# Performance work log

Measured on AMD Instinct MI355X. Metric: run time of the kernel, lower is better.

## Reference

```python
import jax, jax.numpy as jnp
import numpy as np

B, T, C, H = 2, 2048, 1024, 16  # batch, seq (== block_size), n_embd, n_head
HD = C // H  # head dim


def setup_inputs() -> dict:
    key = jax.random.key(0)
    k1, k2, k3 = jax.random.split(key, 3)
    x = jax.random.normal(k1, (B, T, C), dtype=jnp.float32)
    w_attn = jax.random.normal(k2, (C, 3 * C), dtype=jnp.float32) * (1.0 / np.sqrt(C))
    b_attn = jnp.zeros((3 * C,), dtype=jnp.float32)
    w_proj = jax.random.normal(k3, (C, C), dtype=jnp.float32) * (1.0 / np.sqrt(C))
    b_proj = jnp.zeros((C,), dtype=jnp.float32)
    return {"x": x, "w_attn": w_attn, "b_attn": b_attn, "w_proj": w_proj, "b_proj": b_proj}


def reference(x, w_attn, b_attn, w_proj, b_proj):
    # qkv projection: [B,T,3C]
    qkv = x @ w_attn + b_attn
    q, k, v = jnp.split(qkv, 3, axis=-1)
    # -> [B,H,T,HD]
    def to_heads(t):
        return t.reshape(B, T, H, HD).transpose(0, 2, 1, 3)
    q, k, v = to_heads(q), to_heads(k), to_heads(v)
    scale = 1.0 / np.sqrt(HD).astype(np.float32)
    # att: [B,H,T,T]
    att = jnp.einsum("bhqd,bhkd->bhqk", q, k) * scale
    causal = jnp.tril(jnp.ones((T, T), dtype=bool))
    att = jnp.where(causal[None, None], att, -jnp.inf)
    att = jax.nn.softmax(att, axis=-1)
    # y: [B,H,T,HD] -> [B,T,C]
    y = jnp.einsum("bhqk,bhkd->bhqd", att, v)
    y = y.transpose(0, 2, 1, 3).reshape(B, T, C)
    return y @ w_proj + b_proj
```

## Files before the change

kernel.cpp:

```cpp
#include <hip/hip_runtime.h>
#include <stdint.h>

#define Bb 2
#define Tt 2048
#define Cc 1024
#define Hh 16
#define HD 64
#define C3 3072

typedef __bf16 bf16x8 __attribute__((ext_vector_type(8)));
typedef float  f32x4  __attribute__((ext_vector_type(4)));
typedef unsigned short u16;
typedef u16 u16x8 __attribute__((ext_vector_type(8)));
typedef u16 u16x4 __attribute__((ext_vector_type(4)));

#define SCALE2 0.18033688f

__device__ __forceinline__ u16 f2bf(float f) {
  union { float f; unsigned u; } v; v.f = f;
  return (u16)((v.u + 0x7fffu + ((v.u >> 16) & 1u)) >> 16);
}
__device__ __forceinline__ float bf2f(u16 a) {
  union { unsigned u; float f; } v; v.u = ((unsigned)a) << 16; return v.f;
}

__device__ __forceinline__ void gl2lds16(const void* g, void* s) {
  __builtin_amdgcn_global_load_lds(
      (__attribute__((address_space(1))) void*)(g),
      (__attribute__((address_space(3))) void*)(s), 16, 0, 0);
}

__device__ __forceinline__ bf16x8 ldb8(const u16* p) {
  return __builtin_bit_cast(bf16x8, *(const u16x8*)p);
}

__global__ __launch_bounds__(256)
void prep_kernel(const float* __restrict__ x, const float* __restrict__ w_attn,
                 const float* __restrict__ w_proj, u16* __restrict__ xb,
                 u16* __restrict__ wat, u16* __restrict__ wpt) {
  __shared__ u16 tile[64][65];
  const int blk = blockIdx.x;
  const int tid = threadIdx.x;
  if (blk < 4096) {
    int i = blk * 256 + tid;
    float4 v = ((const float4*)x)[i];
    u16x4 o = { f2bf(v.x), f2bf(v.y), f2bf(v.z), f2bf(v.w) };
    ((u16x4*)xb)[i] = o;
    return;
  }
  const float* in; u16* out; int R, C, c0, r0;
  if (blk < 4096 + 768) {
    int t = blk - 4096;
    in = w_attn; out = wat; R = 1024; C = 3072;
    c0 = (t % 48) * 64; r0 = (t / 48) * 64;
  } else {
    int t = blk - 4864;
    in = w_proj; out = wpt; R = 1024; C = 1024;
    c0 = (t & 15) * 64; r0 = (t >> 4) * 64;
  }
  int xx = tid & 63, yy = tid >> 6;
  #pragma unroll
  for (int rr = yy; rr < 64; rr += 4)
    tile[rr][xx] = f2bf(in[(size_t)(r0 + rr) * C + c0 + xx]);
  __syncthreads();
  #pragma unroll
  for (int rr = yy; rr < 64; rr += 4)
    out[(size_t)(c0 + rr) * R + r0 + xx] = tile[xx][rr];
}

template <int MODE, int BN>
__global__ __launch_bounds__(256, 4)
void gemm_bt(const u16* __restrict__ A, const u16* __restrict__ Bt,
             const float* __restrict__ bias, void* __restrict__ Cout,
             u16* __restrict__ Vt, int M, int N, int K) {
  __shared__ u16 As[2][128 * 32];
  __shared__ u16 Bs[2][BN * 32];
  constexpr int JT = BN / 32;
  const int tid = threadIdx.x;
  const int ln  = tid & 63;
  const int w   = tid >> 6;
  const int wm  = w >> 1, wn = w & 1;
  const int l15 = ln & 15, lq = ln >> 4;
  const int swz2 = (l15 >> 1) & 3;
  const int m0 = blockIdx.y * 128, n0 = blockIdx.x * BN;

  int aoff[2], boff[BN / 128 + 1];
  #pragma unroll
  for (int i = 0; i < 2; ++i) {
    int s = i * 256 + tid;
    int row = s >> 2, cg = (s & 3) ^ ((s >> 3) & 3);
    aoff[i] = (m0 + row) * K + cg * 8;
  }
  #pragma unroll
  for (int i = 0; i < BN / 128 + 1; ++i) {
    int s = i * 256 + tid;
    int row = s >> 2, cg = (s & 3) ^ ((s >> 3) & 3);
    boff[i] = (n0 + row) * K + cg * 8;
  }

  f32x4 acc[4][JT];
  #pragma unroll
  for (int i = 0; i < 4; ++i)
    #pragma unroll
    for (int j = 0; j < JT; ++j)
      acc[i][j] = (f32x4){0.f, 0.f, 0.f, 0.f};

  const int NK = K >> 5;
  #pragma unroll
  for (int i = 0; i < 2; ++i)
    gl2lds16(A + aoff[i], (char*)As[0] + (size_t)(i * 256 + w * 64) * 16);
  #pragma unroll
  for (int i = 0; i < BN / 128 + 1; ++i)
    gl2lds16(Bt + boff[i], (char*)Bs[0] + (size_t)(i * 256 + w * 64) * 16);

  for (int it = 0; it < NK; ++it) {
    const int p = it & 1;
    __syncthreads();
    if (it + 1 < NK) {
      const int k0 = (it + 1) * 32;
      #pragma unroll
      for (int i = 0; i < 2; ++i)
        gl2lds16(A + aoff[i] + k0, (char*)As[p ^ 1] + (size_t)(i * 256 + w * 64) * 16);
      #pragma unroll
      for (int i = 0; i < BN / 128 + 1; ++i)
        gl2lds16(Bt + boff[i] + k0, (char*)Bs[p ^ 1] + (size_t)(i * 256 + w * 64) * 16);
    }
    const u16* AsB = As[p];
    const u16* BsB = Bs[p];
    bf16x8 af[4], bfr[JT];
    #pragma unroll
    for (int i = 0; i < 4; ++i)
      af[i] = ldb8(&AsB[(wm * 64 + i * 16 + l15) * 32 + ((lq ^ swz2) * 8)]);
    #pragma unroll
    for (int j = 0; j < JT; ++j)
      bfr[j] = ldb8(&BsB[(wn * (BN / 2) + j * 16 + l15) * 32 + ((lq ^ swz2) * 8)]);
    #pragma unroll
    for (int i = 0; i < 4; ++i)
      #pragma unroll
      for (int j = 0; j < JT; ++j)
        acc[i][j] = __builtin_amdgcn_mfma_f32_16x16x32_bf16(af[i], bfr[j], acc[i][j], 0, 0, 0);
  }

  if (MODE == 1 && n0 >= 2048) {
    #pragma unroll
    for (int i = 0; i < 4; ++i) {
      int rowb = m0 + wm * 64 + i * 16 + lq * 4;
      int b_ = rowb >> 11, t0 = rowb & 2047;
      int tl = t0 & 63;
      int c = tl >> 4, ll = (tl >> 2) & 3;
      int pos0 = (c >> 1) * 32 + ll * 8 + (c & 1) * 4;
      size_t tdst = (size_t)(t0 & ~63) + pos0;
      #pragma unroll
      for (int j = 0; j < JT; ++j) {
        int col = n0 + wn * (BN / 2) + j * 16 + l15;
        int hd = col - 2048;
        float bsv = bias[col];
        u16x4 pk;
        #pragma unroll
        for (int r = 0; r < 4; ++r) pk[r] = f2bf(acc[i][j][r] + bsv);
        *(u16x4*)&Vt[(size_t)(b_ * 1024 + hd) * Tt + tdst] = pk;
      }
    }
  } else {
    const int ldc = (MODE == 1) ? 2048 : N;
    #pragma unroll
    for (int i = 0; i < 4; ++i) {
      int row = m0 + wm * 64 + i * 16 + lq * 4;
      #pragma unroll
      for (int j = 0; j < JT; ++j) {
        int col = n0 + wn * (BN / 2) + j * 16 + l15;
        float bsv = bias[col];
        #pragma unroll
        for (int r = 0; r < 4; ++r) {
          float v = acc[i][j][r] + bsv;
          if (MODE == 1) ((u16*)Cout)[(size_t)(row + r) * ldc + col] = f2bf(v);
          else           ((float*)Cout)[(size_t)(row + r) * ldc + col] = v;
        }
      }
    }
  }
}


__device__ __forceinline__ bf16x8 packp(const f32x4& a, const f32x4& b) {
  bf16x8 r;
  #pragma unroll
  for (int i = 0; i < 4; ++i) { r[i] = (__bf16)a[i]; r[i + 4] = (__bf16)b[i]; }
  return r;
}
__device__ __forceinline__ bf16x8 qscale(const u16* p) {
  u16x8 q = *(const u16x8*)p;
  u16x8 s;
  #pragma unroll
  for (int j = 0; j < 8; ++j) s[j] = f2bf(bf2f(q[j]) * SCALE2);
  return __builtin_bit_cast(bf16x8, s);
}

__global__ __launch_bounds__(256, 4)
void attn_fused(const u16* __restrict__ qk, const u16* __restrict__ vt,
                u16* __restrict__ y) {
  __shared__ u16 Ks[2][64 * 64];
  __shared__ u16 Vts[2][64 * 64];
  const int tid = threadIdx.x;
  const int ln = tid & 63, w = tid >> 6;
  const int l15 = ln & 15, lq = ln >> 4;
  const int swz = l15 & 7;
  const int bx = blockIdx.x;
  const int bh = bx & 31;
  const int h  = bh & 15, b = bh >> 4;
  const int pr = bx >> 5;

  const u16* qbase = qk + (size_t)(b * Tt) * 2048 + h * HD;
  const u16* kbase = qk + (size_t)(b * Tt) * 2048 + 1024 + h * HD;
  const u16* vbase = vt + (size_t)(b * 1024 + h * HD) * Tt;

  const int s0 = tid, s1 = 256 + tid;
  const int koff0 = (s0 >> 3) * 2048 + (((s0 & 7) ^ ((s0 >> 3) & 7)) * 8);
  const int koff1 = (s1 >> 3) * 2048 + (((s1 & 7) ^ ((s1 >> 3) & 7)) * 8);

  gl2lds16(kbase + koff0, (char*)Ks[0] + w * 1024);
  gl2lds16(kbase + koff1, (char*)Ks[0] + 4096 + w * 1024);
  gl2lds16(vbase + koff0, (char*)Vts[0] + w * 1024);
  gl2lds16(vbase + koff1, (char*)Vts[0] + 4096 + w * 1024);

  int pb = 0;

  #pragma unroll
  for (int half = 0; half < 2; ++half) {
    const int qt = half ? pr : 31 - pr;
    const int q0 = qt * 64;
    const int q0w = q0 + w * 16;

    const u16* qrA = qbase + (size_t)(q0w + l15) * 2048;
    bf16x8 qA0 = qscale(qrA + lq * 8), qA1 = qscale(qrA + 32 + lq * 8);

    f32x4 o[4];
    #pragma unroll
    for (int j = 0; j < 4; ++j) o[j] = (f32x4){0, 0, 0, 0};
    float m = -__builtin_inff(), l = 0.f;
    const int qg = q0w + l15;
    const int nkv = qt + 1;

    for (int it = 0; it < nkv; ++it) {
      const int kk = it * 64;
      const int p = pb ^ (it & 1);
      __syncthreads();
      if (it + 1 < nkv) {
        const u16* ksrc = kbase + (size_t)(kk + 64) * 2048;
        const u16* vsrc = vbase + kk + 64;
        gl2lds16(ksrc + koff0, (char*)Ks[p ^ 1] + w * 1024);
        gl2lds16(ksrc + koff1, (char*)Ks[p ^ 1] + 4096 + w * 1024);
        gl2lds16(vsrc + koff0, (char*)Vts[p ^ 1] + w * 1024);
        gl2lds16(vsrc + koff1, (char*)Vts[p ^ 1] + 4096 + w * 1024);
      } else if (half == 0) {
        gl2lds16(kbase + koff0, (char*)Ks[p ^ 1] + w * 1024);
        gl2lds16(kbase + koff1, (char*)Ks[p ^ 1] + 4096 + w * 1024);
        gl2lds16(vbase + koff0, (char*)Vts[p ^ 1] + w * 1024);
        gl2lds16(vbase + koff1, (char*)Vts[p ^ 1] + 4096 + w * 1024);
      }
      const u16* KsB  = Ks[p];
      const u16* VtsB = Vts[p];

      f32x4 t[4];
      #pragma unroll
      for (int i = 0; i < 4; ++i) t[i] = (f32x4){0, 0, 0, 0};
      __builtin_amdgcn_s_setprio(1);
      #pragma unroll
      for (int i = 0; i < 4; ++i) {
        bf16x8 kf0 = ldb8(&KsB[(i * 16 + l15) * 64 + ((lq    ) ^ swz) * 8]);
        bf16x8 kf1 = ldb8(&KsB[(i * 16 + l15) * 64 + ((lq + 4) ^ swz) * 8]);
        t[i] = __builtin_amdgcn_mfma_f32_16x16x32_bf16(kf0, qA0, t[i], 0, 0, 0);
        t[i] = __builtin_amdgcn_mfma_f32_16x16x32_bf16(kf1, qA1, t[i], 0, 0, 0);
      }
      __builtin_amdgcn_s_setprio(0);

      if (it == nkv - 1) {
        #pragma unroll
        for (int i = 0; i < 4; ++i)
          #pragma unroll
          for (int r = 0; r < 4; ++r) {
            int kv = kk + i * 16 + lq * 4 + r;
            if (kv > qg) t[i][r] = -__builtin_inff();
          }
      }

      float a0 = fmaxf(fmaxf(t[0][0], t[0][1]), fmaxf(t[0][2], t[0][3]));
      float a1 = fmaxf(fmaxf(t[1][0], t[1][1]), fmaxf(t[1][2], t[1][3]));
      float a2 = fmaxf(fmaxf(t[2][0], t[2][1]), fmaxf(t[2][2], t[2][3]));
      float a3 = fmaxf(fmaxf(t[3][0], t[3][1]), fmaxf(t[3][2], t[3][3]));
      float mx = fmaxf(fmaxf(a0, a1), fmaxf(a2, a3));
      mx = fmaxf(mx, __shfl_xor(mx, 16));
      mx = fmaxf(mx, __shfl_xor(mx, 32));

      if (!__all(mx <= m + 8.0f)) {
        float mn = fmaxf(m, mx);
        float al = __builtin_amdgcn_exp2f(m - mn);
        m = mn;
        l *= al;
        #pragma unroll
        for (int jd = 0; jd < 4; ++jd)
          #pragma unroll
          for (int r = 0; r < 4; ++r) o[jd][r] *= al;
      }

      #pragma unroll
      for (int i = 0; i < 4; ++i)
        #pragma unroll
        for (int r = 0; r < 4; ++r)
          t[i][r] = __builtin_amdgcn_exp2f(t[i][r] - m);
      float b0 = (t[0][0] + t[0][1]) + (t[0][2] + t[0][3]);
      float b1 = (t[1][0] + t[1][1]) + (t[1][2] + t[1][3]);
      float b2 = (t[2][0] + t[2][1]) + (t[2][2] + t[2][3]);
      float b3 = (t[3][0] + t[3][1]) + (t[3][2] + t[3][3]);
      float ps = (b0 + b1) + (b2 + b3);
      ps += __shfl_xor(ps, 16);
      ps += __shfl_xor(ps, 32);
      l += ps;

      bf16x8 p0 = packp(t[0], t[1]), p1 = packp(t[2], t[3]);
      __builtin_amdgcn_s_setprio(1);
      #pragma unroll
      for (int mf = 0; mf < 2; ++mf) {
        bf16x8 pbv = mf ? p1 : p0;
        #pragma unroll
        for (int jd = 0; jd < 4; ++jd) {
          int d = jd * 16 + l15;
          bf16x8 vf = ldb8(&VtsB[d * 64 + ((mf * 4 + lq) ^ swz) * 8]);
          o[jd] = __builtin_amdgcn_mfma_f32_16x16x32_bf16(vf, pbv, o[jd], 0, 0, 0);
        }
      }
      __builtin_amdgcn_s_setprio(0);
    }
    pb ^= (nkv & 1);

    float inv = 1.f / l;
    const size_t ybase = (size_t)(b * Tt + q0w + l15) * Cc + h * HD;
    #pragma unroll
    for (int jd = 0; jd < 4; ++jd) {
      u16x4 pk;
      #pragma unroll
      for (int r = 0; r < 4; ++r) pk[r] = f2bf(o[jd][r] * inv);
      *(u16x4*)&y[ybase + jd * 16 + lq * 4] = pk;
    }
  }
}

extern "C" void kernel_launch(void* const* d_in, const int* in_sizes, int n_in,
                              void* d_out, int out_size, void* d_ws, size_t ws_size,
                              hipStream_t stream) {
  const float* x      = (const float*)d_in[0];
  const float* w_attn = (const float*)d_in[1];
  const float* b_attn = (const float*)d_in[2];
  const float* w_proj = (const float*)d_in[3];
  const float* b_proj = (const float*)d_in[4];
  float* out = (float*)d_out;

  char* ws = (char*)d_ws;
  u16* xb  = (u16*)(ws + 0);
  u16* wat = (u16*)(ws + 8388608);
  u16* wpt = (u16*)(ws + 14680064);
  u16* qkb = (u16*)(ws + 16777216);
  u16* vtb = (u16*)(ws + 33554432);
  u16* yb  = (u16*)(ws + 41943040);

  prep_kernel<<<5120, 256, 0, stream>>>(x, w_attn, w_proj, xb, wat, wpt);
  gemm_bt<1, 128><<<dim3(24, 32), 256, 0, stream>>>(xb, wat, b_attn, (void*)qkb, vtb, 4096, 3072, 1024);
  attn_fused<<<512, 256, 0, stream>>>(qkb, vtb, yb);
  gemm_bt<0, 64><<<dim3(16, 32), 256, 0, stream>>>(yb, wpt, b_proj, (void*)out, nullptr, 4096, 1024, 1024);
}
```

Baseline: 176.4 us.

## Process paired query tiles concurrently sharing each K/V tile load

```diff
diff --git a/kernel.cpp b/kernel.cpp
--- a/kernel.cpp
+++ b/kernel.cpp
@@ -196,7 +196,52 @@
   return __builtin_bit_cast(bf16x8, s);
 }
 
-__global__ __launch_bounds__(256, 4)
+__device__ __forceinline__ void softmax_step(f32x4 (&t)[4], float& m, f32x4 (&o)[4],
+                                             f32x4& lacc, bool maskDiag, int kk,
+                                             int qg, int lq) {
+  if (maskDiag) {
+    #pragma unroll
+    for (int i = 0; i < 4; ++i)
+      #pragma unroll
+      for (int r = 0; r < 4; ++r) {
+        int kv = kk + i * 16 + lq * 4 + r;
+        if (kv > qg) t[i][r] = -__builtin_inff();
+      }
+  }
+  float a0 = fmaxf(fmaxf(t[0][0], t[0][1]), fmaxf(t[0][2], t[0][3]));
+  float a1 = fmaxf(fmaxf(t[1][0], t[1][1]), fmaxf(t[1][2], t[1][3]));
+  float a2 = fmaxf(fmaxf(t[2][0], t[2][1]), fmaxf(t[2][2], t[2][3]));
+  float a3 = fmaxf(fmaxf(t[3][0], t[3][1]), fmaxf(t[3][2], t[3][3]));
+  float mx = fmaxf(fmaxf(a0, a1), fmaxf(a2, a3));
+  mx = fmaxf(mx, __shfl_xor(mx, 16));
+#if __has_builtin(__builtin_amdgcn_permlane32_swap)
+  {
+    unsigned mu = __builtin_bit_cast(unsigned, mx);
+    auto r2 = __builtin_amdgcn_permlane32_swap(mu, mu, false, false);
+    mx = fmaxf(__builtin_bit_cast(float, (unsigned)r2[0]),
+               __builtin_bit_cast(float, (unsigned)r2[1]));
+  }
+#else
+  mx = fmaxf(mx, __shfl_xor(mx, 32));
+#endif
+  if (!__all(mx <= m + 8.0f)) {
+    float mn = fmaxf(m, mx);
+    float al = __builtin_amdgcn_exp2f(m - mn);
+    m = mn;
+    lacc[0] *= al;
+    #pragma unroll
+    for (int jd = 0; jd < 4; ++jd)
+      #pragma unroll
+      for (int r = 0; r < 4; ++r) o[jd][r] *= al;
+  }
+  #pragma unroll
+  for (int i = 0; i < 4; ++i)
+    #pragma unroll
+    for (int r = 0; r < 4; ++r)
+      t[i][r] = __builtin_amdgcn_exp2f(t[i][r] - m);
+}
+
+__global__ __launch_bounds__(256, 2)
 void attn_fused(const u16* __restrict__ qk, const u16* __restrict__ vt,
                 u16* __restrict__ y) {
   __shared__ u16 Ks[2][64 * 64];
@@ -208,7 +253,9 @@
   const int bx = blockIdx.x;
   const int bh = bx & 31;
   const int h  = bh & 15, b = bh >> 4;
-  const int pr = bx >> 5;
+  const int g  = (bx >> 5) & 7;
+  const int pr = (bx < 256) ? g : 15 - g;
+  const int qtA = 31 - pr, qtB = pr;
 
   const u16* qbase = qk + (size_t)(b * Tt) * 2048 + h * HD;
   const u16* kbase = qk + (size_t)(b * Tt) * 2048 + 1024 + h * HD;
@@ -217,129 +264,113 @@
   const int s0 = tid, s1 = 256 + tid;
   const int koff0 = (s0 >> 3) * 2048 + (((s0 & 7) ^ ((s0 >> 3) & 7)) * 8);
   const int koff1 = (s1 >> 3) * 2048 + (((s1 & 7) ^ ((s1 >> 3) & 7)) * 8);
+
+  const int q0A = qtA * 64 + w * 16;
+  const int q0B = qtB * 64 + w * 16;
+
+  const u16* qrA = qbase + (size_t)(q0A + l15) * 2048;
+  const u16* qrB = qbase + (size_t)(q0B + l15) * 2048;
+  bf16x8 qA0 = qscale(qrA + lq * 8), qA1 = qscale(qrA + 32 + lq * 8);
+  bf16x8 qB0 = qscale(qrB + lq * 8), qB1 = qscale(qrB + 32 + lq * 8);
+
+  bf16x8 ones;
+  #pragma unroll
+  for (int j = 0; j < 8; ++j) ones[j] = (__bf16)1.0f;
+
+  f32x4 oA[4], oB[4];
+  #pragma unroll
+  for (int j = 0; j < 4; ++j) { oA[j] = (f32x4){0, 0, 0, 0}; oB[j] = (f32x4){0, 0, 0, 0}; }
+  f32x4 laccA = (f32x4){0, 0, 0, 0}, laccB = (f32x4){0, 0, 0, 0};
+  float mA = -__builtin_inff(), mB = -__builtin_inff();
+  const int qgA = q0A + l15, qgB = q0B + l15;
+
+  const int itLast = qtA;
 
   gl2lds16(kbase + koff0, (char*)Ks[0] + w * 1024);
   gl2lds16(kbase + koff1, (char*)Ks[0] + 4096 + w * 1024);
   gl2lds16(vbase + koff0, (char*)Vts[0] + w * 1024);
   gl2lds16(vbase + koff1, (char*)Vts[0] + 4096 + w * 1024);
 
-  int pb = 0;
-
-  #pragma unroll
-  for (int half = 0; half < 2; ++half) {
-    const int qt = half ? pr : 31 - pr;
-    const int q0 = qt * 64;
-    const int q0w = q0 + w * 16;
-
-    const u16* qrA = qbase + (size_t)(q0w + l15) * 2048;
-    bf16x8 qA0 = qscale(qrA + lq * 8), qA1 = qscale(qrA + 32 + lq * 8);
-
-    f32x4 o[4];
-    #pragma unroll
-    for (int j = 0; j < 4; ++j) o[j] = (f32x4){0, 0, 0, 0};
-    float m = -__builtin_inff(), l = 0.f;
-    const int qg = q0w + l15;
-    const int nkv = qt + 1;
-
-    for (int it = 0; it < nkv; ++it) {
-      const int kk = it * 64;
-      const int p = pb ^ (it & 1);
-      __syncthreads();
-      if (it + 1 < nkv) {
-        const u16* ksrc = kbase + (size_t)(kk + 64) * 2048;
-        const u16* vsrc = vbase + kk + 64;
-        gl2lds16(ksrc + koff0, (char*)Ks[p ^ 1] + w * 1024);
-        gl2lds16(ksrc + koff1, (char*)Ks[p ^ 1] + 4096 + w * 1024);
-        gl2lds16(vsrc + koff0, (char*)Vts[p ^ 1] + w * 1024);
-        gl2lds16(vsrc + koff1, (char*)Vts[p ^ 1] + 4096 + w * 1024);
-      } else if (half == 0) {
-        gl2lds16(kbase + koff0, (char*)Ks[p ^ 1] + w * 1024);
-        gl2lds16(kbase + koff1, (char*)Ks[p ^ 1] + 4096 + w * 1024);
-        gl2lds16(vbase + koff0, (char*)Vts[p ^ 1] + w * 1024);
-        gl2lds16(vbase + koff1, (char*)Vts[p ^ 1] + 4096 + w * 1024);
+  for (int it = 0; it <= itLast; ++it) {
+    const int kk = it * 64;
+    const int p = it & 1;
+    __syncthreads();
+    if (it < itLast) {
+      const u16* ksrc = kbase + (size_t)(kk + 64) * 2048;
+      const u16* vsrc = vbase + kk + 64;
+      gl2lds16(ksrc + koff0, (char*)Ks[p ^ 1] + w * 1024);
+      gl2lds16(ksrc + koff1, (char*)Ks[p ^ 1] + 4096 + w * 1024);
+      gl2lds16(vsrc + koff0, (char*)Vts[p ^ 1] + w * 1024);
+      gl2lds16(vsrc + koff1, (char*)Vts[p ^ 1] + 4096 + w * 1024);
+    }
+    const u16* KsB  = Ks[p];
+    const u16* VtsB = Vts[p];
+    const bool actB = (it <= qtB);
+
+    f32x4 tA[4], tB[4];
+    #pragma unroll
+    for (int i = 0; i < 4; ++i) { tA[i] = (f32x4){0, 0, 0, 0}; tB[i] = (f32x4){0, 0, 0, 0}; }
+    __builtin_amdgcn_s_setprio(1);
+    #pragma unroll
+    for (int i = 0; i < 4; ++i) {
+      bf16x8 kf0 = ldb8(&KsB[(i * 16 + l15) * 64 + ((lq    ) ^ swz) * 8]);
+      bf16x8 kf1 = ldb8(&KsB[(i * 16 + l15) * 64 + ((lq + 4) ^ swz) * 8]);
+      tA[i] = __builtin_amdgcn_mfma_f32_16x16x32_bf16(kf0, qA0, tA[i], 0, 0, 0);
+      tA[i] = __builtin_amdgcn_mfma_f32_16x16x32_bf16(kf1, qA1, tA[i], 0, 0, 0);
+      if (actB) {
+        tB[i] = __builtin_amdgcn_mfma_f32_16x16x32_bf16(kf0, qB0, tB[i], 0, 0, 0);
+        tB[i] = __builtin_amdgcn_mfma_f32_16x16x32_bf16(kf1, qB1, tB[i], 0, 0, 0);
       }
-      const u16* KsB  = Ks[p];
-      const u16* VtsB = Vts[p];
-
-      f32x4 t[4];
-      #pragma unroll
-      for (int i = 0; i < 4; ++i) t[i] = (f32x4){0, 0, 0, 0};
-      __builtin_amdgcn_s_setprio(1);
-      #pragma unroll
-      for (int i = 0; i < 4; ++i) {
-        bf16x8 kf0 = ldb8(&KsB[(i * 16 + l15) * 64 + ((lq    ) ^ swz) * 8]);
-        bf16x8 kf1 = ldb8(&KsB[(i * 16 + l15) * 64 + ((lq + 4) ^ swz) * 8]);
-        t[i] = __builtin_amdgcn_mfma_f32_16x16x32_bf16(kf0, qA0, t[i], 0, 0, 0);
-        t[i] = __builtin_amdgcn_mfma_f32_16x16x32_bf16(kf1, qA1, t[i], 0, 0, 0);
+    }
+    __builtin_amdgcn_s_setprio(0);
+
+    softmax_step(tA, mA, oA, laccA, it == itLast, kk, qgA, lq);
+    bf16x8 pA0 = packp(tA[0], tA[1]), pA1 = packp(tA[2], tA[3]);
+    bf16x8 pB0 = {}, pB1 = {};
+    if (actB) {
+      softmax_step(tB, mB, oB, laccB, it == qtB, kk, qgB, lq);
+      pB0 = packp(tB[0], tB[1]); pB1 = packp(tB[2], tB[3]);
+    }
+
+    __builtin_amdgcn_s_setprio(1);
+    #pragma unroll
+    for (int mf = 0; mf < 2; ++mf) {
+      bf16x8 pa = mf ? pA1 : pA0;
+      bf16x8 pb = mf ? pB1 : pB0;
+      laccA = __builtin_amdgcn_mfma_f32_16x16x32_bf16(ones, pa, laccA, 0, 0, 0);
+      if (actB)
+        laccB = __builtin_amdgcn_mfma_f32_16x16x32_bf16(ones, pb, laccB, 0, 0, 0);
+      #pragma unroll
+      for (int jd = 0; jd < 4; ++jd) {
+        int d = jd * 16 + l15;
+        bf16x8 vf = ldb8(&VtsB[d * 64 + ((mf * 4 + lq) ^ swz) * 8]);
+        oA[jd] = __builtin_amdgcn_mfma_f32_16x16x32_bf16(vf, pa, oA[jd], 0, 0, 0);
+        if (actB)
+          oB[jd] = __builtin_amdgcn_mfma_f32_16x16x32_bf16(vf, pb, oB[jd], 0, 0, 0);
       }
-      __builtin_amdgcn_s_setprio(0);
-
-      if (it == nkv - 1) {
-        #pragma unroll
-        for (int i = 0; i < 4; ++i)
-          #pragma unroll
-          for (int r = 0; r < 4; ++r) {
-            int kv = kk + i * 16 + lq * 4 + r;
-            if (kv > qg) t[i][r] = -__builtin_inff();
-          }
-      }
-
-      float a0 = fmaxf(fmaxf(t[0][0], t[0][1]), fmaxf(t[0][2], t[0][3]));
-      float a1 = fmaxf(fmaxf(t[1][0], t[1][1]), fmaxf(t[1][2], t[1][3]));
-      float a2 = fmaxf(fmaxf(t[2][0], t[2][1]), fmaxf(t[2][2], t[2][3]));
-      float a3 = fmaxf(fmaxf(t[3][0], t[3][1]), fmaxf(t[3][2], t[3][3]));
-      float mx = fmaxf(fmaxf(a0, a1), fmaxf(a2, a3));
-      mx = fmaxf(mx, __shfl_xor(mx, 16));
-      mx = fmaxf(mx, __shfl_xor(mx, 32));
-
-      if (!__all(mx <= m + 8.0f)) {
-        float mn = fmaxf(m, mx);
-        float al = __builtin_amdgcn_exp2f(m - mn);
-        m = mn;
-        l *= al;
-        #pragma unroll
-        for (int jd = 0; jd < 4; ++jd)
-          #pragma unroll
-          for (int r = 0; r < 4; ++r) o[jd][r] *= al;
-      }
-
-      #pragma unroll
-      for (int i = 0; i < 4; ++i)
-        #pragma unroll
-        for (int r = 0; r < 4; ++r)
-          t[i][r] = __builtin_amdgcn_exp2f(t[i][r] - m);
-      float b0 = (t[0][0] + t[0][1]) + (t[0][2] + t[0][3]);
-      float b1 = (t[1][0] + t[1][1]) + (t[1][2] + t[1][3]);
-      float b2 = (t[2][0] + t[2][1]) + (t[2][2] + t[2][3]);
-      float b3 = (t[3][0] + t[3][1]) + (t[3][2] + t[3][3]);
-      float ps = (b0 + b1) + (b2 + b3);
-      ps += __shfl_xor(ps, 16);
-      ps += __shfl_xor(ps, 32);
-      l += ps;
-
-      bf16x8 p0 = packp(t[0], t[1]), p1 = packp(t[2], t[3]);
-      __builtin_amdgcn_s_setprio(1);
-      #pragma unroll
-      for (int mf = 0; mf < 2; ++mf) {
-        bf16x8 pbv = mf ? p1 : p0;
-        #pragma unroll
-        for (int jd = 0; jd < 4; ++jd) {
-          int d = jd * 16 + l15;
-          bf16x8 vf = ldb8(&VtsB[d * 64 + ((mf * 4 + lq) ^ swz) * 8]);
-          o[jd] = __builtin_amdgcn_mfma_f32_16x16x32_bf16(vf, pbv, o[jd], 0, 0, 0);
-        }
-      }
-      __builtin_amdgcn_s_setprio(0);
-    }
-    pb ^= (nkv & 1);
-
-    float inv = 1.f / l;
-    const size_t ybase = (size_t)(b * Tt + q0w + l15) * Cc + h * HD;
+    }
+    __builtin_amdgcn_s_setprio(0);
+  }
+
+  {
+    float inv = 1.f / laccA[0];
+    const size_t ybase = (size_t)(b * Tt + q0A + l15) * Cc + h * HD;
     #pragma unroll
     for (int jd = 0; jd < 4; ++jd) {
       u16x4 pk;
       #pragma unroll
-      for (int r = 0; r < 4; ++r) pk[r] = f2bf(o[jd][r] * inv);
+      for (int r = 0; r < 4; ++r) pk[r] = f2bf(oA[jd][r] * inv);
+      *(u16x4*)&y[ybase + jd * 16 + lq * 4] = pk;
+    }
+  }
+  {
+    float inv = 1.f / laccB[0];
+    const size_t ybase = (size_t)(b * Tt + q0B + l15) * Cc + h * HD;
+    #pragma unroll
+    for (int jd = 0; jd < 4; ++jd) {
+      u16x4 pk;
+      #pragma unroll
+      for (int r = 0; r < 4; ++r) pk[r] = f2bf(oB[jd][r] * inv);
       *(u16x4*)&y[ybase + jd * 16 + lq * 4] = pk;
     }
   }
```

Result: slower. 186.7 us (+5.8%).

## Triple-buffer GEMM and attention loads, split attention blocks, MFMA row-sum

Applied to the files above, without the earlier changes.

```diff
diff --git a/kernel.cpp b/kernel.cpp
--- a/kernel.cpp
+++ b/kernel.cpp
@@ -32,6 +32,15 @@
 
 __device__ __forceinline__ bf16x8 ldb8(const u16* p) {
   return __builtin_bit_cast(bf16x8, *(const u16x8*)p);
+}
+
+template <int N>
+__device__ __forceinline__ void vmwait() {
+  asm volatile("s_waitcnt vmcnt(%0)" :: "n"(N) : "memory");
+}
+__device__ __forceinline__ void barrier_nodrain() {
+  __builtin_amdgcn_s_barrier();
+  __builtin_amdgcn_sched_barrier(0);
 }
 
 __global__ __launch_bounds__(256)
@@ -68,14 +77,16 @@
     out[(size_t)(c0 + rr) * R + r0 + xx] = tile[xx][rr];
 }
 
-template <int MODE, int BN>
-__global__ __launch_bounds__(256, 4)
+template <int MODE, int BN, int MINW>
+__global__ __launch_bounds__(256, MINW)
 void gemm_bt(const u16* __restrict__ A, const u16* __restrict__ Bt,
              const float* __restrict__ bias, void* __restrict__ Cout,
              u16* __restrict__ Vt, int M, int N, int K) {
-  __shared__ u16 As[2][128 * 32];
-  __shared__ u16 Bs[2][BN * 32];
+  __shared__ u16 As[3][128 * 32];
+  __shared__ u16 Bs[3][BN * 32];
   constexpr int JT = BN / 32;
+  constexpr int NB = BN / 128 + 1;
+  constexpr int L  = 2 + NB;
   const int tid = threadIdx.x;
   const int ln  = tid & 63;
   const int w   = tid >> 6;
@@ -84,7 +95,7 @@
   const int swz2 = (l15 >> 1) & 3;
   const int m0 = blockIdx.y * 128, n0 = blockIdx.x * BN;
 
-  int aoff[2], boff[BN / 128 + 1];
+  int aoff[2], boff[NB];
   #pragma unroll
   for (int i = 0; i < 2; ++i) {
     int s = i * 256 + tid;
@@ -92,7 +103,7 @@
     aoff[i] = (m0 + row) * K + cg * 8;
   }
   #pragma unroll
-  for (int i = 0; i < BN / 128 + 1; ++i) {
+  for (int i = 0; i < NB; ++i) {
     int s = i * 256 + tid;
     int row = s >> 2, cg = (s & 3) ^ ((s >> 3) & 3);
     boff[i] = (n0 + row) * K + cg * 8;
@@ -106,27 +117,27 @@
       acc[i][j] = (f32x4){0.f, 0.f, 0.f, 0.f};
 
   const int NK = K >> 5;
-  #pragma unroll
-  for (int i = 0; i < 2; ++i)
-    gl2lds16(A + aoff[i], (char*)As[0] + (size_t)(i * 256 + w * 64) * 16);
-  #pragma unroll
-  for (int i = 0; i < BN / 128 + 1; ++i)
-    gl2lds16(Bt + boff[i], (char*)Bs[0] + (size_t)(i * 256 + w * 64) * 16);
-
+
+  auto STAGE = [&](int buf, int t) {
+    const int k0 = t * 32;
+    #pragma unroll
+    for (int i = 0; i < 2; ++i)
+      gl2lds16(A + aoff[i] + k0, (char*)As[buf] + (size_t)(i * 256 + w * 64) * 16);
+    #pragma unroll
+    for (int i = 0; i < NB; ++i)
+      gl2lds16(Bt + boff[i] + k0, (char*)Bs[buf] + (size_t)(i * 256 + w * 64) * 16);
+  };
+
+  STAGE(0, 0);
+  if (NK > 1) STAGE(1, 1);
+
+  int cur = 0;
   for (int it = 0; it < NK; ++it) {
-    const int p = it & 1;
-    __syncthreads();
-    if (it + 1 < NK) {
-      const int k0 = (it + 1) * 32;
-      #pragma unroll
-      for (int i = 0; i < 2; ++i)
-        gl2lds16(A + aoff[i] + k0, (char*)As[p ^ 1] + (size_t)(i * 256 + w * 64) * 16);
-      #pragma unroll
-      for (int i = 0; i < BN / 128 + 1; ++i)
-        gl2lds16(Bt + boff[i] + k0, (char*)Bs[p ^ 1] + (size_t)(i * 256 + w * 64) * 16);
-    }
-    const u16* AsB = As[p];
-    const u16* BsB = Bs[p];
+    if (it + 1 < NK) vmwait<L>(); else vmwait<0>();
+    barrier_nodrain();
+    if (it + 2 < NK) STAGE(cur == 0 ? 2 : cur - 1, it + 2);
+    const u16* AsB = As[cur];
+    const u16* BsB = Bs[cur];
     bf16x8 af[4], bfr[JT];
     #pragma unroll
     for (int i = 0; i < 4; ++i)
@@ -139,6 +150,7 @@
       #pragma unroll
       for (int j = 0; j < JT; ++j)
         acc[i][j] = __builtin_amdgcn_mfma_f32_16x16x32_bf16(af[i], bfr[j], acc[i][j], 0, 0, 0);
+    cur = (cur == 2) ? 0 : cur + 1;
   }
 
   if (MODE == 1 && n0 >= 2048) {
@@ -196,11 +208,56 @@
   return __builtin_bit_cast(bf16x8, s);
 }
 
-__global__ __launch_bounds__(256, 4)
+__device__ __forceinline__ void softmax_step(f32x4 (&t)[4], float& m, f32x4 (&o)[4],
+                                             f32x4& lacc, bool maskDiag, int kk,
+                                             int qg, int lq) {
+  if (maskDiag) {
+    #pragma unroll
+    for (int i = 0; i < 4; ++i)
+      #pragma unroll
+      for (int r = 0; r < 4; ++r) {
+        int kv = kk + i * 16 + lq * 4 + r;
+        if (kv > qg) t[i][r] = -__builtin_inff();
+      }
+  }
+  float a0 = fmaxf(fmaxf(t[0][0], t[0][1]), fmaxf(t[0][2], t[0][3]));
+  float a1 = fmaxf(fmaxf(t[1][0], t[1][1]), fmaxf(t[1][2], t[1][3]));
+  float a2 = fmaxf(fmaxf(t[2][0], t[2][1]), fmaxf(t[2][2], t[2][3]));
+  float a3 = fmaxf(fmaxf(t[3][0], t[3][1]), fmaxf(t[3][2], t[3][3]));
+  float mx = fmaxf(fmaxf(a0, a1), fmaxf(a2, a3));
+  mx = fmaxf(mx, __shfl_xor(mx, 16));
+#if __has_builtin(__builtin_amdgcn_permlane32_swap)
+  {
+    unsigned mu = __builtin_bit_cast(unsigned, mx);
+    auto r2 = __builtin_amdgcn_permlane32_swap(mu, mu, false, false);
+    mx = fmaxf(__builtin_bit_cast(float, (unsigned)r2[0]),
+               __builtin_bit_cast(float, (unsigned)r2[1]));
+  }
+#else
+  mx = fmaxf(mx, __shfl_xor(mx, 32));
+#endif
+  if (!__all(mx <= m + 8.0f)) {
+    float mn = fmaxf(m, mx);
+    float al = __builtin_amdgcn_exp2f(m - mn);
+    m = mn;
+    lacc[0] *= al;
+    #pragma unroll
+    for (int jd = 0; jd < 4; ++jd)
+      #pragma unroll
+      for (int r = 0; r < 4; ++r) o[jd][r] *= al;
+  }
+  #pragma unroll
+  for (int i = 0; i < 4; ++i)
+    #pragma unroll
+    for (int r = 0; r < 4; ++r)
+      t[i][r] = __builtin_amdgcn_exp2f(t[i][r] - m);
+}
+
+__global__ __launch_bounds__(256, 3)
 void attn_fused(const u16* __restrict__ qk, const u16* __restrict__ vt,
                 u16* __restrict__ y) {
-  __shared__ u16 Ks[2][64 * 64];
-  __shared__ u16 Vts[2][64 * 64];
+  __shared__ u16 Ks[3][64 * 64];
+  __shared__ u16 Vts[3][64 * 64];
   const int tid = threadIdx.x;
   const int ln = tid & 63, w = tid >> 6;
   const int l15 = ln & 15, lq = ln >> 4;
@@ -208,7 +265,9 @@
   const int bx = blockIdx.x;
   const int bh = bx & 31;
   const int h  = bh & 15, b = bh >> 4;
-  const int pr = bx >> 5;
+  const int rr_ = bx >> 8, g = (bx >> 5) & 7;
+  const int qt = (rr_ == 0) ? 31 - g : (rr_ == 1) ? 16 + g : (rr_ == 2) ? 15 - g : g;
+  const int q0w = qt * 64 + w * 16;
 
   const u16* qbase = qk + (size_t)(b * Tt) * 2048 + h * HD;
   const u16* kbase = qk + (size_t)(b * Tt) * 2048 + 1024 + h * HD;
@@ -218,130 +277,82 @@
   const int koff0 = (s0 >> 3) * 2048 + (((s0 & 7) ^ ((s0 >> 3) & 7)) * 8);
   const int koff1 = (s1 >> 3) * 2048 + (((s1 & 7) ^ ((s1 >> 3) & 7)) * 8);
 
-  gl2lds16(kbase + koff0, (char*)Ks[0] + w * 1024);
-  gl2lds16(kbase + koff1, (char*)Ks[0] + 4096 + w * 1024);
-  gl2lds16(vbase + koff0, (char*)Vts[0] + w * 1024);
-  gl2lds16(vbase + koff1, (char*)Vts[0] + 4096 + w * 1024);
-
-  int pb = 0;
-
-  #pragma unroll
-  for (int half = 0; half < 2; ++half) {
-    const int qt = half ? pr : 31 - pr;
-    const int q0 = qt * 64;
-    const int q0w = q0 + w * 16;
-
-    const u16* qrA = qbase + (size_t)(q0w + l15) * 2048;
-    bf16x8 qA0 = qscale(qrA + lq * 8), qA1 = qscale(qrA + 32 + lq * 8);
-
-    f32x4 o[4];
-    #pragma unroll
-    for (int j = 0; j < 4; ++j) o[j] = (f32x4){0, 0, 0, 0};
-    float m = -__builtin_inff(), l = 0.f;
-    const int qg = q0w + l15;
-    const int nkv = qt + 1;
-
-    for (int it = 0; it < nkv; ++it) {
-      const int kk = it * 64;
-      const int p = pb ^ (it & 1);
-      __syncthreads();
-      if (it + 1 < nkv) {
-        const u16* ksrc = kbase + (size_t)(kk + 64) * 2048;
-        const u16* vsrc = vbase + kk + 64;
-        gl2lds16(ksrc + koff0, (char*)Ks[p ^ 1] + w * 1024);
-        gl2lds16(ksrc + koff1, (char*)Ks[p ^ 1] + 4096 + w * 1024);
-        gl2lds16(vsrc + koff0, (char*)Vts[p ^ 1] + w * 1024);
-        gl2lds16(vsrc + koff1, (char*)Vts[p ^ 1] + 4096 + w * 1024);
-      } else if (half == 0) {
-        gl2lds16(kbase + koff0, (char*)Ks[p ^ 1] + w * 1024);
-        gl2lds16(kbase + koff1, (char*)Ks[p ^ 1] + 4096 + w * 1024);
-        gl2lds16(vbase + koff0, (char*)Vts[p ^ 1] + w * 1024);
-        gl2lds16(vbase + koff1, (char*)Vts[p ^ 1] + 4096 + w * 1024);
+  const u16* qrA = qbase + (size_t)(q0w + l15) * 2048;
+  bf16x8 qA0 = qscale(qrA + lq * 8), qA1 = qscale(qrA + 32 + lq * 8);
+
+  bf16x8 ones;
+  #pragma unroll
+  for (int j = 0; j < 8; ++j) ones[j] = (__bf16)1.0f;
+
+  f32x4 o[4];
+  #pragma unroll
+  for (int j = 0; j < 4; ++j) o[j] = (f32x4){0, 0, 0, 0};
+  f32x4 lacc = (f32x4){0, 0, 0, 0};
+  float m = -__builtin_inff();
+  const int qg = q0w + l15;
+  const int nkv = qt + 1;
+
+  auto STAGE = [&](int buf, int t) {
+    const u16* ks = kbase + (size_t)(t * 64) * 2048;
+    const u16* vs = vbase + t * 64;
+    gl2lds16(ks + koff0, (char*)Ks[buf] + w * 1024);
+    gl2lds16(ks + koff1, (char*)Ks[buf] + 4096 + w * 1024);
+    gl2lds16(vs + koff0, (char*)Vts[buf] + w * 1024);
+    gl2lds16(vs + koff1, (char*)Vts[buf] + 4096 + w * 1024);
+  };
+
+  STAGE(0, 0);
+  if (nkv > 1) STAGE(1, 1);
+
+  int cur = 0;
+  for (int it = 0; it < nkv; ++it) {
+    const int kk = it * 64;
+    if (it + 1 < nkv) vmwait<4>(); else vmwait<0>();
+    barrier_nodrain();
+    if (it + 2 < nkv) STAGE(cur == 0 ? 2 : cur - 1, it + 2);
+    const u16* KsB  = Ks[cur];
+    const u16* VtsB = Vts[cur];
+
+    f32x4 t[4];
+    #pragma unroll
+    for (int i = 0; i < 4; ++i) t[i] = (f32x4){0, 0, 0, 0};
+    __builtin_amdgcn_s_setprio(1);
+    #pragma unroll
+    for (int i = 0; i < 4; ++i) {
+      bf16x8 kf0 = ldb8(&KsB[(i * 16 + l15) * 64 + ((lq    ) ^ swz) * 8]);
+      bf16x8 kf1 = ldb8(&KsB[(i * 16 + l15) * 64 + ((lq + 4) ^ swz) * 8]);
+      t[i] = __builtin_amdgcn_mfma_f32_16x16x32_bf16(kf0, qA0, t[i], 0, 0, 0);
+      t[i] = __builtin_amdgcn_mfma_f32_16x16x32_bf16(kf1, qA1, t[i], 0, 0, 0);
+    }
+    __builtin_amdgcn_s_setprio(0);
+
+    softmax_step(t, m, o, lacc, it == nkv - 1, kk, qg, lq);
+    bf16x8 p0 = packp(t[0], t[1]), p1 = packp(t[2], t[3]);
+
+    __builtin_amdgcn_s_setprio(1);
+    #pragma unroll
+    for (int mf = 0; mf < 2; ++mf) {
+      bf16x8 pbv = mf ? p1 : p0;
+      lacc = __builtin_amdgcn_mfma_f32_16x16x32_bf16(ones, pbv, lacc, 0, 0, 0);
+      #pragma unroll
+      for (int jd = 0; jd < 4; ++jd) {
+        int d = jd * 16 + l15;
+        bf16x8 vf = ldb8(&VtsB[d * 64 + ((mf * 4 + lq) ^ swz) * 8]);
+        o[jd] = __builtin_amdgcn_mfma_f32_16x16x32_bf16(vf, pbv, o[jd], 0, 0, 0);
       }
-      const u16* KsB  = Ks[p];
-      const u16* VtsB = Vts[p];
-
-      f32x4 t[4];
-      #pragma unroll
-      for (int i = 0; i < 4; ++i) t[i] = (f32x4){0, 0, 0, 0};
-      __builtin_amdgcn_s_setprio(1);
-      #pragma unroll
-      for (int i = 0; i < 4; ++i) {
-        bf16x8 kf0 = ldb8(&KsB[(i * 16 + l15) * 64 + ((lq    ) ^ swz) * 8]);
-        bf16x8 kf1 = ldb8(&KsB[(i * 16 + l15) * 64 + ((lq + 4) ^ swz) * 8]);
-        t[i] = __builtin_amdgcn_mfma_f32_16x16x32_bf16(kf0, qA0, t[i], 0, 0, 0);
-        t[i] = __builtin_amdgcn_mfma_f32_16x16x32_bf16(kf1, qA1, t[i], 0, 0, 0);
-      }
-      __builtin_amdgcn_s_setprio(0);
-
-      if (it == nkv - 1) {
-        #pragma unroll
-        for (int i = 0; i < 4; ++i)
-          #pragma unroll
-          for (int r = 0; r < 4; ++r) {
-            int kv = kk + i * 16 + lq * 4 + r;
-            if (kv > qg) t[i][r] = -__builtin_inff();
-          }
-      }
-
-      float a0 = fmaxf(fmaxf(t[0][0], t[0][1]), fmaxf(t[0][2], t[0][3]));
-      float a1 = fmaxf(fmaxf(t[1][0], t[1][1]), fmaxf(t[1][2], t[1][3]));
-      float a2 = fmaxf(fmaxf(t[2][0], t[2][1]), fmaxf(t[2][2], t[2][3]));
-      float a3 = fmaxf(fmaxf(t[3][0], t[3][1]), fmaxf(t[3][2], t[3][3]));
-      float mx = fmaxf(fmaxf(a0, a1), fmaxf(a2, a3));
-      mx = fmaxf(mx, __shfl_xor(mx, 16));
-      mx = fmaxf(mx, __shfl_xor(mx, 32));
-
-      if (!__all(mx <= m + 8.0f)) {
-        float mn = fmaxf(m, mx);
-        float al = __builtin_amdgcn_exp2f(m - mn);
-        m = mn;
-        l *= al;
-        #pragma unroll
-        for (int jd = 0; jd < 4; ++jd)
-          #pragma unroll
-          for (int r = 0; r < 4; ++r) o[jd][r] *= al;
-      }
-
-      #pragma unroll
-      for (int i = 0; i < 4; ++i)
-        #pragma unroll
-        for (int r = 0; r < 4; ++r)
-          t[i][r] = __builtin_amdgcn_exp2f(t[i][r] - m);
-      float b0 = (t[0][0] + t[0][1]) + (t[0][2] + t[0][3]);
-      float b1 = (t[1][0] + t[1][1]) + (t[1][2] + t[1][3]);
-      float b2 = (t[2][0] + t[2][1]) + (t[2][2] + t[2][3]);
-      float b3 = (t[3][0] + t[3][1]) + (t[3][2] + t[3][3]);
-      float ps = (b0 + b1) + (b2 + b3);
-      ps += __shfl_xor(ps, 16);
-      ps += __shfl_xor(ps, 32);
-      l += ps;
-
-      bf16x8 p0 = packp(t[0], t[1]), p1 = packp(t[2], t[3]);
-      __builtin_amdgcn_s_setprio(1);
-      #pragma unroll
-      for (int mf = 0; mf < 2; ++mf) {
-        bf16x8 pbv = mf ? p1 : p0;
-        #pragma unroll
-        for (int jd = 0; jd < 4; ++jd) {
-          int d = jd * 16 + l15;
-          bf16x8 vf = ldb8(&VtsB[d * 64 + ((mf * 4 + lq) ^ swz) * 8]);
-          o[jd] = __builtin_amdgcn_mfma_f32_16x16x32_bf16(vf, pbv, o[jd], 0, 0, 0);
-        }
-      }
-      __builtin_amdgcn_s_setprio(0);
     }
-    pb ^= (nkv & 1);
-
-    float inv = 1.f / l;
-    const size_t ybase = (size_t)(b * Tt + q0w + l15) * Cc + h * HD;
-    #pragma unroll
-    for (int jd = 0; jd < 4; ++jd) {
-      u16x4 pk;
-      #pragma unroll
-      for (int r = 0; r < 4; ++r) pk[r] = f2bf(o[jd][r] * inv);
-      *(u16x4*)&y[ybase + jd * 16 + lq * 4] = pk;
-    }
+    __builtin_amdgcn_s_setprio(0);
+    cur = (cur == 2) ? 0 : cur + 1;
+  }
+
+  float inv = 1.f / lacc[0];
+  const size_t ybase = (size_t)(b * Tt + q0w + l15) * Cc + h * HD;
+  #pragma unroll
+  for (int jd = 0; jd < 4; ++jd) {
+    u16x4 pk;
+    #pragma unroll
+    for (int r = 0; r < 4; ++r) pk[r] = f2bf(o[jd][r] * inv);
+    *(u16x4*)&y[ybase + jd * 16 + lq * 4] = pk;
   }
 }
 
@@ -364,7 +375,7 @@
   u16* yb  = (u16*)(ws + 41943040);
 
   prep_kernel<<<5120, 256, 0, stream>>>(x, w_attn, w_proj, xb, wat, wpt);
-  gemm_bt<1, 128><<<dim3(24, 32), 256, 0, stream>>>(xb, wat, b_attn, (void*)qkb, vtb, 4096, 3072, 1024);
-  attn_fused<<<512, 256, 0, stream>>>(qkb, vtb, yb);
-  gemm_bt<0, 64><<<dim3(16, 32), 256, 0, stream>>>(yb, wpt, b_proj, (void*)out, nullptr, 4096, 1024, 1024);
-}
+  gemm_bt<1, 128, 3><<<dim3(24, 32), 256, 0, stream>>>(xb, wat, b_attn, (void*)qkb, vtb, 4096, 3072, 1024);
+  attn_fused<<<1024, 256, 0, stream>>>(qkb, vtb, yb);
+  gemm_bt<0, 64, 4><<<dim3(16, 32), 256, 0, stream>>>(yb, wpt, b_proj, (void*)out, nullptr, 4096, 1024, 1024);
+}
```

Measured after the change: 174.5 us. No clear change (-1.1%).
